# Performance work log

Hardware: AMD Instinct MI355X
Metric: run time of the kernel (lower is better)

Reference implementation:

```python
import jax, jax.numpy as jnp
import numpy as np
import math

B, N, DQK, DV, M = 8, 8192, 128, 128, 256


def _make_omega(m: int, d: int, seed: int = 0) -> jnp.ndarray:
    """Block-orthogonal random feature matrix, shape [d, m] (matches torch _omega)."""
    rng = np.random.default_rng(seed)
    blocks = []
    nblocks = m // d
    for _ in range(nblocks):
        q, _ = np.linalg.qr(rng.standard_normal((d, d)))
        blocks.append(q.T)
    missing = m - nblocks * d
    if missing > 0:
        q, _ = np.linalg.qr(rng.standard_normal((d, d)))
        blocks.append(q.T[:missing])
    norm = np.linalg.norm(rng.standard_normal((m, d)), axis=1, keepdims=True)
    omega = (norm * np.vstack(blocks)).T  # [d, m]
    return jnp.asarray(omega, dtype=jnp.float32)


def setup_inputs() -> dict:
    key = jax.random.key(0)
    kq, kk, kv = jax.random.split(key, 3)
    Q = jax.random.normal(kq, (B, N, DQK), jnp.float32)
    K = jax.random.normal(kk, (B, N, DQK), jnp.float32)
    V = jax.random.normal(kv, (B, N, DV), jnp.float32)
    atom_mask = jnp.ones((B, N), jnp.float32)
    omega = _make_omega(M, DQK)
    return {"Q": Q, "K": K, "V": V, "atom_mask": atom_mask, "omega": omega}


def _phi(X, mask, omega, is_query: bool, eps: float = 1e-4):
    """Project into random-feature space with Performer stabilization."""
    d = X.shape[-1]
    m = omega.shape[-1]
    U = (X / d ** 0.25) @ omega                       # [B, N, m]
    h = jnp.sum(X * X, axis=-1, keepdims=True) / (2.0 * d ** 0.5)
    if is_query:
        mx = jnp.max(U, axis=-1, keepdims=True)       # per-token max
    else:
        mx = jnp.max(U, axis=(-2, -1), keepdims=True)  # per-batch max
    return (jnp.exp(U - h - mx) + eps) / math.sqrt(m) * mask[..., None]


def reference(Q, K, V, atom_mask, omega):
    eps = 1e-8
    Qp = _phi(Q, atom_mask, omega, True)   # [B, N, M]
    Kp = _phi(K, atom_mask, omega, False)  # [B, N, M]
    # norm_n = Qp_n . sum_j Kp_j
    norm = jnp.einsum('bnm,bm->bn', Qp, jnp.sum(Kp, axis=1))[..., None] + eps
    KV = jnp.einsum('bnm,bnv->bmv', Kp, V)             # [B, M, DV]
    return jnp.einsum('bnm,bmv->bnv', Qp, KV) / norm   # [B, N, DV]
```

## Files before the change

kernel.cpp:

```cpp
#include <hip/hip_runtime.h>
#include <math.h>

#define BB 8
#define NN 8192
#define DD 128
#define MM 256
#define DVV 128
#define PP 32
#define CHUNK 32

#define XSCALE 0.29730177875068026f
#define INV_SQRT_M 0.0625f

typedef _Float16 f16x8 __attribute__((ext_vector_type(8)));
typedef float f32x16 __attribute__((ext_vector_type(16)));

#define FR(s, l) ((s) * 520 + (l) * 8)

__device__ __forceinline__ unsigned f2ord(float f) {
    unsigned u = __float_as_uint(f);
    return (u & 0x80000000u) ? ~u : (u | 0x80000000u);
}
__device__ __forceinline__ float ord2f(unsigned u) {
    return (u & 0x80000000u) ? __uint_as_float(u & 0x7fffffffu) : __uint_as_float(~u);
}
__device__ __forceinline__ f32x16 mfma16(f16x8 a, f16x8 b, f32x16 c) {
    return __builtin_amdgcn_mfma_f32_32x32x16_f16(a, b, c, 0, 0, 0);
}
__device__ __forceinline__ int rowf(int r, int q) { return (r & 3) + 8 * (r >> 2) + 4 * q; }

__device__ __forceinline__ void stage_A(const float* __restrict__ src,
                                        _Float16* R1, float* hs, float* msk,
                                        const float* __restrict__ mrow, bool do_h) {
    const int tid = threadIdx.x;
    const int t = tid >> 3, ks = tid & 7;
    const float4* s4 = (const float4*)(src + t * DD + ks * 16);
    float x[16];
    #pragma unroll
    for (int u = 0; u < 4; ++u) {
        float4 v = s4[u];
        x[u*4+0] = v.x * XSCALE; x[u*4+1] = v.y * XSCALE;
        x[u*4+2] = v.z * XSCALE; x[u*4+3] = v.w * XSCALE;
    }
    if (do_h) {
        float p = 0.f;
        #pragma unroll
        for (int u = 0; u < 16; ++u) p += x[u] * x[u];
        p += __shfl_xor(p, 1, 64); p += __shfl_xor(p, 2, 64); p += __shfl_xor(p, 4, 64);
        if (ks == 0) { hs[t] = 0.5f * p; msk[t] = mrow[t]; }
    }
    #pragma unroll
    for (int q = 0; q < 2; ++q) {
        f16x8 h8, l8;
        #pragma unroll
        for (int j = 0; j < 8; ++j) {
            float xv = x[q*8 + j];
            _Float16 h = (_Float16)xv;
            h8[j] = h; l8[j] = (_Float16)(xv - (float)h);
        }
        *(f16x8*)&R1[FR(0*8 + ks, q*32 + t)] = h8;
        *(f16x8*)&R1[FR(1*8 + ks, q*32 + t)] = l8;
    }
}

__device__ __forceinline__ void stage_BV(const float* __restrict__ src, _Float16* R1) {
    const int tid = threadIdx.x;
    const int t = tid >> 3, c0 = (tid & 7) * 16;
    const int ts = t >> 4, qq = (t >> 3) & 1, j = t & 7;
    const float4* s4 = (const float4*)(src + t * DVV + c0);
    #pragma unroll
    for (int u = 0; u < 4; ++u) {
        float4 v = s4[u];
        float vv[4] = {v.x, v.y, v.z, v.w};
        #pragma unroll
        for (int e = 0; e < 4; ++e) {
            int c = c0 + u*4 + e;
            int vt = c >> 5, iv = c & 31;
            _Float16 h = (_Float16)vv[e];
            R1[FR((0*4 + vt)*2 + ts, qq*32 + iv) + j] = h;
            R1[FR((1*4 + vt)*2 + ts, qq*32 + iv) + j] = (_Float16)(vv[e] - (float)h);
        }
    }
}

__global__ __launch_bounds__(256) void pack_kernel(const float* __restrict__ omega,
                                                   _Float16* __restrict__ omh,
                                                   _Float16* __restrict__ oml,
                                                   unsigned* __restrict__ kmaxord) {
    int g = blockIdx.x * 256 + threadIdx.x;
    if (g < BB) kmaxord[g] = f2ord(-INFINITY);
    int lane = g & 63, ks = (g >> 6) & 7, nt = g >> 9;
    int q = lane >> 5, i = lane & 31;
    f16x8 h8, l8;
    #pragma unroll
    for (int j = 0; j < 8; ++j) {
        float w = omega[(size_t)(ks*16 + q*8 + j) * MM + nt*32 + i];
        _Float16 h = (_Float16)w;
        h8[j] = h; l8[j] = (_Float16)(w - (float)h);
    }
    ((f16x8*)omh)[g] = h8;
    ((f16x8*)oml)[g] = l8;
}

__global__ __launch_bounds__(256) void kmax_kernel(const float* __restrict__ K,
                                                   const _Float16* __restrict__ omh,
                                                   unsigned* __restrict__ kmaxord) {
    __shared__ __align__(16) _Float16 R1[16 * 520];
    __shared__ float wred[4];
    const int b = blockIdx.y;
    const int tid = threadIdx.x, w = tid >> 6, lane = tid & 63;

    f16x8 om[2][8];
    #pragma unroll
    for (int n = 0; n < 2; ++n)
        #pragma unroll
        for (int k = 0; k < 8; ++k)
            om[n][k] = ((const f16x8*)omh)[((2*w + n)*8 + k)*64 + lane];

    float mx = -INFINITY;
    for (int c = 0; c < 4; ++c) {
        int t0 = (blockIdx.x * 4 + c) * CHUNK;
        __syncthreads();
        stage_A(K + ((size_t)b*NN + t0) * DD, R1, nullptr, nullptr, nullptr, false);
        __syncthreads();
        f32x16 a0, a1;
        #pragma unroll
        for (int r = 0; r < 16; ++r) { a0[r] = 0.f; a1[r] = 0.f; }
        #pragma unroll
        for (int ks = 0; ks < 8; ++ks) {
            f16x8 ah = *(const f16x8*)&R1[FR(ks, lane)];
            a0 = mfma16(ah, om[0][ks], a0);
            a1 = mfma16(ah, om[1][ks], a1);
        }
        #pragma unroll
        for (int r = 0; r < 16; ++r) mx = fmaxf(mx, fmaxf(a0[r], a1[r]));
    }
    #pragma unroll
    for (int off = 1; off < 64; off <<= 1) mx = fmaxf(mx, __shfl_xor(mx, off, 64));
    if (lane == 0) wred[w] = mx;
    __syncthreads();
    if (tid == 0)
        atomicMax(kmaxord + b,
                  f2ord(fmaxf(fmaxf(wred[0], wred[1]), fmaxf(wred[2], wred[3]))));
}

__global__ __launch_bounds__(256) void kv_kernel(const float* __restrict__ K,
                                                 const float* __restrict__ V,
                                                 const float* __restrict__ mask,
                                                 const _Float16* __restrict__ omh,
                                                 const _Float16* __restrict__ oml,
                                                 const unsigned* __restrict__ kmaxord,
                                                 float* __restrict__ pkv,
                                                 float* __restrict__ pks) {
    __shared__ __align__(16) _Float16 R1[16 * 520];
    __shared__ __align__(16) _Float16 R2[16 * 520];
    __shared__ float hs[32], msk[32];
    const int b = blockIdx.y, bx = blockIdx.x;
    const int rest = bx >> 3;
    const int h = rest & 1;
    const int p = (rest >> 1) * 8 + (bx & 7);
    const int tid = threadIdx.x, w = tid >> 6, lane = tid & 63;
    const int i = tid & 31, q = (tid >> 5) & 1;
    const int nt = h * 4 + w;
    const float kmaxv = ord2f(kmaxord[b]);

    f16x8 omf[2][8];
    #pragma unroll
    for (int k = 0; k < 8; ++k) {
        omf[0][k] = ((const f16x8*)omh)[(nt*8 + k)*64 + lane];
        omf[1][k] = ((const f16x8*)oml)[(nt*8 + k)*64 + lane];
    }

    f32x16 kvacc[4];
    #pragma unroll
    for (int vt = 0; vt < 4; ++vt)
        #pragma unroll
        for (int r = 0; r < 16; ++r) kvacc[vt][r] = 0.f;
    float ksa = 0.f;

    for (int c = 0; c < 8; ++c) {
        int t0 = (p * 8 + c) * CHUNK;
        __syncthreads();
        stage_A(K + ((size_t)b*NN + t0) * DD, R1, hs, msk,
                mask + (size_t)b*NN + t0, true);
        __syncthreads();

        f32x16 a0;
        #pragma unroll
        for (int r = 0; r < 16; ++r) a0[r] = 0.f;
        #pragma unroll
        for (int ks = 0; ks < 8; ++ks) {
            f16x8 ah = *(const f16x8*)&R1[FR(ks, lane)];
            f16x8 al = *(const f16x8*)&R1[FR(8 + ks, lane)];
            a0 = mfma16(ah, omf[0][ks], a0);
            a0 = mfma16(ah, omf[1][ks], a0);
            a0 = mfma16(al, omf[0][ks], a0);
        }
        __syncthreads();

        stage_BV(V + ((size_t)b*NN + t0) * DVV, R1);
        #pragma unroll
        for (int r = 0; r < 16; ++r) {
            int tok = rowf(r, q);
            float hh = hs[tok] + kmaxv;
            float mm = msk[tok] * INV_SQRT_M;
            float kp = (__expf(a0[r] - hh) + 1e-4f) * mm;
            ksa += kp;
            int ts = tok >> 4, qq = (tok >> 3) & 1, j = tok & 7;
            _Float16 hv = (_Float16)kp;
            R2[FR(w*2 + ts, qq*32 + i) + j] = hv;
            R2[FR(8 + w*2 + ts, qq*32 + i) + j] = (_Float16)(kp - (float)hv);
        }
        __syncthreads();

        f16x8 ah2[2], al2[2];
        #pragma unroll
        for (int ts = 0; ts < 2; ++ts) {
            ah2[ts] = *(const f16x8*)&R2[FR(w*2 + ts, lane)];
            al2[ts] = *(const f16x8*)&R2[FR(8 + w*2 + ts, lane)];
        }
        #pragma unroll
        for (int vt = 0; vt < 4; ++vt) {
            #pragma unroll
            for (int ts = 0; ts < 2; ++ts) {
                f16x8 bh = *(const f16x8*)&R1[FR(vt*2 + ts, lane)];
                f16x8 bl = *(const f16x8*)&R1[FR(8 + vt*2 + ts, lane)];
                kvacc[vt] = mfma16(ah2[ts], bh, kvacc[vt]);
                kvacc[vt] = mfma16(ah2[ts], bl, kvacc[vt]);
                kvacc[vt] = mfma16(al2[ts], bh, kvacc[vt]);
            }
        }
    }

    float* dst = pkv + ((size_t)(b * PP + p) << 15);
    #pragma unroll
    for (int vt = 0; vt < 4; ++vt)
        #pragma unroll
        for (int r = 0; r < 16; ++r) {
            int feat = nt*32 + rowf(r, q);
            dst[feat * DVV + vt*32 + i] = kvacc[vt][r];
        }
    {
        float s = ksa + __shfl_xor(ksa, 32, 64);
        if (q == 0) pks[(size_t)(b * PP + p) * MM + nt*32 + i] = s;
    }
}

__global__ __launch_bounds__(256) void reduce_kernel(const float* __restrict__ pkv,
                                                     const float* __restrict__ pks,
                                                     float* __restrict__ ksum,
                                                     _Float16* __restrict__ kvph,
                                                     _Float16* __restrict__ kvpl) {
    const int b = blockIdx.y;
    int g = blockIdx.x * 256 + threadIdx.x;
    float s = 0.f;
    for (int p = 0; p < PP; ++p) s += pkv[((size_t)(b * PP + p) << 15) + g];
    int f = g >> 7, v = g & 127;
    int vt = v >> 5, iv = v & 31, fs = f >> 4, qq = (f >> 3) & 1, j = f & 7;
    size_t idx = (size_t)b * 32768 + (size_t)((vt*16 + fs)*64 + qq*32 + iv)*8 + j;
    _Float16 h = (_Float16)s;
    kvph[idx] = h;
    kvpl[idx] = (_Float16)(s - (float)h);
    if (blockIdx.x == 0) {
        float ss = 0.f;
        for (int p = 0; p < PP; ++p) ss += pks[(size_t)(b * PP + p) * MM + g];
        ksum[b * MM + g] = ss;
    }
}

__global__ __launch_bounds__(256) void out_kernel(const float* __restrict__ Q,
                                                  const float* __restrict__ mask,
                                                  const _Float16* __restrict__ omh,
                                                  const _Float16* __restrict__ oml,
                                                  const float* __restrict__ ksum,
                                                  const _Float16* __restrict__ kvph,
                                                  const _Float16* __restrict__ kvpl,
                                                  float* __restrict__ out) {
    __shared__ __align__(16) _Float16 R1[16 * 520];
    __shared__ __align__(16) _Float16 R2[32 * 520];
    __shared__ float hs[32], msk[32], wmax[4][32], norms[32];
    const int b = blockIdx.y;
    const int tid = threadIdx.x, w = tid >> 6, lane = tid & 63;
    const int i = tid & 31, q = (tid >> 5) & 1;

    f16x8 omf[2][2][8];
    #pragma unroll
    for (int n = 0; n < 2; ++n)
        #pragma unroll
        for (int k = 0; k < 8; ++k) {
            omf[0][n][k] = ((const f16x8*)omh)[((2*w + n)*8 + k)*64 + lane];
            omf[1][n][k] = ((const f16x8*)oml)[((2*w + n)*8 + k)*64 + lane];
        }
    f16x8 bfh[16], bfl[16];
    #pragma unroll
    for (int fs = 0; fs < 16; ++fs) {
        bfh[fs] = ((const f16x8*)kvph)[(size_t)b * 4096 + (w*16 + fs)*64 + lane];
        bfl[fs] = ((const f16x8*)kvpl)[(size_t)b * 4096 + (w*16 + fs)*64 + lane];
    }
    f16x8 bnh[4], bnl[4];
    #pragma unroll
    for (int u = 0; u < 4; ++u) {
        f16x8 hh, ll;
        #pragma unroll
        for (int j = 0; j < 8; ++j) { hh[j] = (_Float16)0.f; ll[j] = (_Float16)0.f; }
        if (i == 0) {
            #pragma unroll
            for (int j = 0; j < 8; ++j) {
                float s = ksum[b * MM + (4*w + u)*16 + q*8 + j];
                _Float16 h = (_Float16)s;
                hh[j] = h; ll[j] = (_Float16)(s - (float)h);
            }
        }
        bnh[u] = hh; bnl[u] = ll;
    }

    for (int c = 0; c < 4; ++c) {
        int t0 = (blockIdx.x * 4 + c) * CHUNK;
        __syncthreads();
        stage_A(Q + ((size_t)b*NN + t0) * DD, R1, hs, msk,
                mask + (size_t)b*NN + t0, true);
        if (tid < 32) norms[tid] = 1e-8f;
        __syncthreads();

        f32x16 a0, a1;
        #pragma unroll
        for (int r = 0; r < 16; ++r) { a0[r] = 0.f; a1[r] = 0.f; }
        #pragma unroll
        for (int ks = 0; ks < 8; ++ks) {
            f16x8 ah = *(const f16x8*)&R1[FR(ks, lane)];
            f16x8 al = *(const f16x8*)&R1[FR(8 + ks, lane)];
            a0 = mfma16(ah, omf[0][0][ks], a0);
            a0 = mfma16(ah, omf[1][0][ks], a0);
            a0 = mfma16(al, omf[0][0][ks], a0);
            a1 = mfma16(ah, omf[0][1][ks], a1);
            a1 = mfma16(ah, omf[1][1][ks], a1);
            a1 = mfma16(al, omf[0][1][ks], a1);
        }
        float tm[16];
        #pragma unroll
        for (int r = 0; r < 16; ++r) tm[r] = fmaxf(a0[r], a1[r]);
        #pragma unroll
        for (int off = 1; off < 32; off <<= 1)
            #pragma unroll
            for (int r = 0; r < 16; ++r) tm[r] = fmaxf(tm[r], __shfl_xor(tm[r], off, 64));
        if (i == 0)
            #pragma unroll
            for (int r = 0; r < 16; ++r) wmax[w][rowf(r, q)] = tm[r];
        __syncthreads();

        #pragma unroll
        for (int r = 0; r < 16; ++r) {
            int tok = rowf(r, q);
            float tmax = fmaxf(fmaxf(wmax[0][tok], wmax[1][tok]),
                               fmaxf(wmax[2][tok], wmax[3][tok]));
            float hh = hs[tok] + tmax;
            float mm = msk[tok] * INV_SQRT_M;
            #pragma unroll
            for (int n = 0; n < 2; ++n) {
                float qp = (__expf((n ? a1[r] : a0[r]) - hh) + 1e-4f) * mm;
                int feat = (2*w + n)*32 + i;
                int fstep = feat >> 4, fq = (i >> 3) & 1, fj = i & 7;
                _Float16 h = (_Float16)qp;
                R2[FR(fstep, fq*32 + tok) + fj] = h;
                R2[FR(16 + fstep, fq*32 + tok) + fj] = (_Float16)(qp - (float)h);
            }
        }
        __syncthreads();

        f32x16 oa, na;
        #pragma unroll
        for (int r = 0; r < 16; ++r) { oa[r] = 0.f; na[r] = 0.f; }
        #pragma unroll
        for (int fs = 0; fs < 16; ++fs) {
            f16x8 ah = *(const f16x8*)&R2[FR(fs, lane)];
            f16x8 al = *(const f16x8*)&R2[FR(16 + fs, lane)];
            oa = mfma16(ah, bfh[fs], oa);
            oa = mfma16(ah, bfl[fs], oa);
            oa = mfma16(al, bfh[fs], oa);
        }
        #pragma unroll
        for (int u = 0; u < 4; ++u) {
            f16x8 ah = *(const f16x8*)&R2[FR(4*w + u, lane)];
            f16x8 al = *(const f16x8*)&R2[FR(16 + 4*w + u, lane)];
            na = mfma16(ah, bnh[u], na);
            na = mfma16(ah, bnl[u], na);
            na = mfma16(al, bnh[u], na);
        }
        if (i == 0)
            #pragma unroll
            for (int r = 0; r < 16; ++r) atomicAdd(&norms[rowf(r, q)], na[r]);
        __syncthreads();

        float* ob = out + ((size_t)b*NN + t0) * DVV + w*32 + i;
        #pragma unroll
        for (int r = 0; r < 16; ++r) {
            int tok = rowf(r, q);
            ob[(size_t)tok * DVV] = oa[r] * __builtin_amdgcn_rcpf(norms[tok]);
        }
    }
}

extern "C" void kernel_launch(void* const* d_in, const int* in_sizes, int n_in,
                              void* d_out, int out_size, void* d_ws, size_t ws_size,
                              hipStream_t stream) {
    const float* Q     = (const float*)d_in[0];
    const float* K     = (const float*)d_in[1];
    const float* V     = (const float*)d_in[2];
    const float* mask  = (const float*)d_in[3];
    const float* omega = (const float*)d_in[4];
    float* out = (float*)d_out;

    char* ws = (char*)d_ws;
    _Float16* omh    = (_Float16*)(ws);
    _Float16* oml    = (_Float16*)(ws + (64 << 10));
    unsigned* kmaxord = (unsigned*)(ws + (128 << 10));
    float*    ksum   = (float*)(ws + (132 << 10));
    float*    pks    = (float*)(ws + (140 << 10));
    _Float16* kvph   = (_Float16*)(ws + (400 << 10));
    _Float16* kvpl   = (_Float16*)(ws + (912 << 10));
    float*    pkv    = (float*)(ws + (2 << 20));

    pack_kernel<<<16, 256, 0, stream>>>(omega, omh, oml, kmaxord);
    kmax_kernel<<<dim3(64, BB), 256, 0, stream>>>(K, omh, kmaxord);
    kv_kernel<<<dim3(64, BB), 256, 0, stream>>>(K, V, mask, omh, oml, kmaxord, pkv, pks);
    reduce_kernel<<<dim3(128, BB), 256, 0, stream>>>(pkv, pks, ksum, kvph, kvpl);
    out_kernel<<<dim3(64, BB), 256, 0, stream>>>(Q, mask, omh, oml, ksum, kvph, kvpl, out);
}
```

Before: 247.1 us.

## Stream omega and KV fragments from global memory instead of holding them in registers

Drops the register-resident omega, KV and ksum fragment arrays in all three kernels. The B operands are now loaded from global/L2 memory inside non-unrolled, software-prefetched (double-buffered) MFMA loops, which should cut VGPR pressure and raise occupancy. In out_kernel the normalizer MFMA pass is replaced by a scalar dot product with ksum followed by a shuffle reduction, and one barrier is removed. The cost is repeated global loads on every chunk, plus less unrolling and less instruction-level parallelism.

```diff
diff --git a/kernel.cpp b/kernel.cpp
--- a/kernel.cpp
+++ b/kernel.cpp
@@ -109,15 +109,11 @@
     __shared__ float wred[4];
     const int b = blockIdx.y;
     const int tid = threadIdx.x, w = tid >> 6, lane = tid & 63;
-
-    f16x8 om[2][8];
-    #pragma unroll
-    for (int n = 0; n < 2; ++n)
-        #pragma unroll
-        for (int k = 0; k < 8; ++k)
-            om[n][k] = ((const f16x8*)omh)[((2*w + n)*8 + k)*64 + lane];
+    const int w2 = 2 * w;
+    const f16x8* OH = (const f16x8*)omh;
 
     float mx = -INFINITY;
+    #pragma unroll 1
     for (int c = 0; c < 4; ++c) {
         int t0 = (blockIdx.x * 4 + c) * CHUNK;
         __syncthreads();
@@ -126,11 +122,21 @@
         f32x16 a0, a1;
         #pragma unroll
         for (int r = 0; r < 16; ++r) { a0[r] = 0.f; a1[r] = 0.f; }
-        #pragma unroll
-        for (int ks = 0; ks < 8; ++ks) {
+        f16x8 X0 = OH[(w2*8 + 0)*64 + lane];
+        f16x8 X1 = OH[((w2+1)*8 + 0)*64 + lane];
+        #pragma unroll 1
+        for (int ks = 0; ks < 8; ks += 2) {
+            f16x8 Y0 = OH[(w2*8 + ks + 1)*64 + lane];
+            f16x8 Y1 = OH[((w2+1)*8 + ks + 1)*64 + lane];
             f16x8 ah = *(const f16x8*)&R1[FR(ks, lane)];
-            a0 = mfma16(ah, om[0][ks], a0);
-            a1 = mfma16(ah, om[1][ks], a1);
+            a0 = mfma16(ah, X0, a0);
+            a1 = mfma16(ah, X1, a1);
+            int k2 = (ks + 2) & 7;
+            X0 = OH[(w2*8 + k2)*64 + lane];
+            X1 = OH[((w2+1)*8 + k2)*64 + lane];
+            f16x8 ah2 = *(const f16x8*)&R1[FR(ks + 1, lane)];
+            a0 = mfma16(ah2, Y0, a0);
+            a1 = mfma16(ah2, Y1, a1);
         }
         #pragma unroll
         for (int r = 0; r < 16; ++r) mx = fmaxf(mx, fmaxf(a0[r], a1[r]));
@@ -163,13 +169,8 @@
     const int i = tid & 31, q = (tid >> 5) & 1;
     const int nt = h * 4 + w;
     const float kmaxv = ord2f(kmaxord[b]);
-
-    f16x8 omf[2][8];
-    #pragma unroll
-    for (int k = 0; k < 8; ++k) {
-        omf[0][k] = ((const f16x8*)omh)[(nt*8 + k)*64 + lane];
-        omf[1][k] = ((const f16x8*)oml)[(nt*8 + k)*64 + lane];
-    }
+    const f16x8* OH = (const f16x8*)omh;
+    const f16x8* OL = (const f16x8*)oml;
 
     f32x16 kvacc[4];
     #pragma unroll
@@ -178,6 +179,7 @@
         for (int r = 0; r < 16; ++r) kvacc[vt][r] = 0.f;
     float ksa = 0.f;
 
+    #pragma unroll 1
     for (int c = 0; c < 8; ++c) {
         int t0 = (p * 8 + c) * CHUNK;
         __syncthreads();
@@ -188,13 +190,25 @@
         f32x16 a0;
         #pragma unroll
         for (int r = 0; r < 16; ++r) a0[r] = 0.f;
-        #pragma unroll
-        for (int ks = 0; ks < 8; ++ks) {
+        f16x8 Xh = OH[(nt*8 + 0)*64 + lane];
+        f16x8 Xl = OL[(nt*8 + 0)*64 + lane];
+        #pragma unroll 1
+        for (int ks = 0; ks < 8; ks += 2) {
+            f16x8 Yh = OH[(nt*8 + ks + 1)*64 + lane];
+            f16x8 Yl = OL[(nt*8 + ks + 1)*64 + lane];
             f16x8 ah = *(const f16x8*)&R1[FR(ks, lane)];
             f16x8 al = *(const f16x8*)&R1[FR(8 + ks, lane)];
-            a0 = mfma16(ah, omf[0][ks], a0);
-            a0 = mfma16(ah, omf[1][ks], a0);
-            a0 = mfma16(al, omf[0][ks], a0);
+            a0 = mfma16(ah, Xh, a0);
+            a0 = mfma16(ah, Xl, a0);
+            a0 = mfma16(al, Xh, a0);
+            int k2 = (ks + 2) & 7;
+            Xh = OH[(nt*8 + k2)*64 + lane];
+            Xl = OL[(nt*8 + k2)*64 + lane];
+            f16x8 ah2 = *(const f16x8*)&R1[FR(ks + 1, lane)];
+            f16x8 al2 = *(const f16x8*)&R1[FR(8 + ks + 1, lane)];
+            a0 = mfma16(ah2, Yh, a0);
+            a0 = mfma16(ah2, Yl, a0);
+            a0 = mfma16(al2, Yh, a0);
         }
         __syncthreads();
 
@@ -282,38 +296,15 @@
     const int b = blockIdx.y;
     const int tid = threadIdx.x, w = tid >> 6, lane = tid & 63;
     const int i = tid & 31, q = (tid >> 5) & 1;
-
-    f16x8 omf[2][2][8];
-    #pragma unroll
-    for (int n = 0; n < 2; ++n)
-        #pragma unroll
-        for (int k = 0; k < 8; ++k) {
-            omf[0][n][k] = ((const f16x8*)omh)[((2*w + n)*8 + k)*64 + lane];
-            omf[1][n][k] = ((const f16x8*)oml)[((2*w + n)*8 + k)*64 + lane];
-        }
-    f16x8 bfh[16], bfl[16];
-    #pragma unroll
-    for (int fs = 0; fs < 16; ++fs) {
-        bfh[fs] = ((const f16x8*)kvph)[(size_t)b * 4096 + (w*16 + fs)*64 + lane];
-        bfl[fs] = ((const f16x8*)kvpl)[(size_t)b * 4096 + (w*16 + fs)*64 + lane];
-    }
-    f16x8 bnh[4], bnl[4];
-    #pragma unroll
-    for (int u = 0; u < 4; ++u) {
-        f16x8 hh, ll;
-        #pragma unroll
-        for (int j = 0; j < 8; ++j) { hh[j] = (_Float16)0.f; ll[j] = (_Float16)0.f; }
-        if (i == 0) {
-            #pragma unroll
-            for (int j = 0; j < 8; ++j) {
-                float s = ksum[b * MM + (4*w + u)*16 + q*8 + j];
-                _Float16 h = (_Float16)s;
-                hh[j] = h; ll[j] = (_Float16)(s - (float)h);
-            }
-        }
-        bnh[u] = hh; bnl[u] = ll;
-    }
-
+    const int w2 = 2 * w;
+    const f16x8* OH = (const f16x8*)omh;
+    const f16x8* OL = (const f16x8*)oml;
+    const f16x8* KH = (const f16x8*)kvph + (size_t)b * 4096 + (w*16)*64 + lane;
+    const f16x8* KL = (const f16x8*)kvpl + (size_t)b * 4096 + (w*16)*64 + lane;
+    const float nk0 = ksum[b * MM + w2*32 + i];
+    const float nk1 = ksum[b * MM + (w2+1)*32 + i];
+
+    #pragma unroll 1
     for (int c = 0; c < 4; ++c) {
         int t0 = (blockIdx.x * 4 + c) * CHUNK;
         __syncthreads();
@@ -325,17 +316,25 @@
         f32x16 a0, a1;
         #pragma unroll
         for (int r = 0; r < 16; ++r) { a0[r] = 0.f; a1[r] = 0.f; }
-        #pragma unroll
-        for (int ks = 0; ks < 8; ++ks) {
+        f16x8 X0h = OH[(w2*8 + 0)*64 + lane], X0l = OL[(w2*8 + 0)*64 + lane];
+        f16x8 X1h = OH[((w2+1)*8 + 0)*64 + lane], X1l = OL[((w2+1)*8 + 0)*64 + lane];
+        #pragma unroll 1
+        for (int ks = 0; ks < 8; ks += 2) {
+            f16x8 Y0h = OH[(w2*8 + ks + 1)*64 + lane], Y0l = OL[(w2*8 + ks + 1)*64 + lane];
+            f16x8 Y1h = OH[((w2+1)*8 + ks + 1)*64 + lane], Y1l = OL[((w2+1)*8 + ks + 1)*64 + lane];
             f16x8 ah = *(const f16x8*)&R1[FR(ks, lane)];
             f16x8 al = *(const f16x8*)&R1[FR(8 + ks, lane)];
-            a0 = mfma16(ah, omf[0][0][ks], a0);
-            a0 = mfma16(ah, omf[1][0][ks], a0);
-            a0 = mfma16(al, omf[0][0][ks], a0);
-            a1 = mfma16(ah, omf[0][1][ks], a1);
-            a1 = mfma16(ah, omf[1][1][ks], a1);
-            a1 = mfma16(al, omf[0][1][ks], a1);
-        }
+            a0 = mfma16(ah, X0h, a0); a0 = mfma16(ah, X0l, a0); a0 = mfma16(al, X0h, a0);
+            a1 = mfma16(ah, X1h, a1); a1 = mfma16(ah, X1l, a1); a1 = mfma16(al, X1h, a1);
+            int k2 = (ks + 2) & 7;
+            X0h = OH[(w2*8 + k2)*64 + lane]; X0l = OL[(w2*8 + k2)*64 + lane];
+            X1h = OH[((w2+1)*8 + k2)*64 + lane]; X1l = OL[((w2+1)*8 + k2)*64 + lane];
+            f16x8 ah2 = *(const f16x8*)&R1[FR(ks + 1, lane)];
+            f16x8 al2 = *(const f16x8*)&R1[FR(8 + ks + 1, lane)];
+            a0 = mfma16(ah2, Y0h, a0); a0 = mfma16(ah2, Y0l, a0); a0 = mfma16(al2, Y0h, a0);
+            a1 = mfma16(ah2, Y1h, a1); a1 = mfma16(ah2, Y1l, a1); a1 = mfma16(al2, Y1h, a1);
+        }
+
         float tm[16];
         #pragma unroll
         for (int r = 0; r < 16; ++r) tm[r] = fmaxf(a0[r], a1[r]);
@@ -348,6 +347,7 @@
             for (int r = 0; r < 16; ++r) wmax[w][rowf(r, q)] = tm[r];
         __syncthreads();
 
+        float nacc[16];
         #pragma unroll
         for (int r = 0; r < 16; ++r) {
             int tok = rowf(r, q);
@@ -355,41 +355,49 @@
                                fmaxf(wmax[2][tok], wmax[3][tok]));
             float hh = hs[tok] + tmax;
             float mm = msk[tok] * INV_SQRT_M;
+            float qp0 = (__expf(a0[r] - hh) + 1e-4f) * mm;
+            float qp1 = (__expf(a1[r] - hh) + 1e-4f) * mm;
+            nacc[r] = qp0 * nk0 + qp1 * nk1;
+            {
+                int feat = w2*32 + i;
+                int fstep = feat >> 4, fq = (i >> 3) & 1, fj = i & 7;
+                _Float16 hv = (_Float16)qp0;
+                R2[FR(fstep, fq*32 + tok) + fj] = hv;
+                R2[FR(16 + fstep, fq*32 + tok) + fj] = (_Float16)(qp0 - (float)hv);
+            }
+            {
+                int feat = (w2+1)*32 + i;
+                int fstep = feat >> 4, fq = (i >> 3) & 1, fj = i & 7;
+                _Float16 hv = (_Float16)qp1;
+                R2[FR(fstep, fq*32 + tok) + fj] = hv;
+                R2[FR(16 + fstep, fq*32 + tok) + fj] = (_Float16)(qp1 - (float)hv);
+            }
+        }
+        #pragma unroll
+        for (int off = 1; off < 32; off <<= 1)
             #pragma unroll
-            for (int n = 0; n < 2; ++n) {
-                float qp = (__expf((n ? a1[r] : a0[r]) - hh) + 1e-4f) * mm;
-                int feat = (2*w + n)*32 + i;
-                int fstep = feat >> 4, fq = (i >> 3) & 1, fj = i & 7;
-                _Float16 h = (_Float16)qp;
-                R2[FR(fstep, fq*32 + tok) + fj] = h;
-                R2[FR(16 + fstep, fq*32 + tok) + fj] = (_Float16)(qp - (float)h);
-            }
-        }
-        __syncthreads();
-
-        f32x16 oa, na;
-        #pragma unroll
-        for (int r = 0; r < 16; ++r) { oa[r] = 0.f; na[r] = 0.f; }
-        #pragma unroll
-        for (int fs = 0; fs < 16; ++fs) {
+            for (int r = 0; r < 16; ++r) nacc[r] += __shfl_xor(nacc[r], off, 64);
+        if (i == 0)
+            #pragma unroll
+            for (int r = 0; r < 16; ++r) atomicAdd(&norms[rowf(r, q)], nacc[r]);
+        __syncthreads();
+
+        f32x16 oa;
+        #pragma unroll
+        for (int r = 0; r < 16; ++r) oa[r] = 0.f;
+        f16x8 Fh = KH[0], Fl = KL[0];
+        #pragma unroll 1
+        for (int fs = 0; fs < 16; fs += 2) {
+            f16x8 Gh = KH[(fs + 1)*64], Gl = KL[(fs + 1)*64];
             f16x8 ah = *(const f16x8*)&R2[FR(fs, lane)];
             f16x8 al = *(const f16x8*)&R2[FR(16 + fs, lane)];
-            oa = mfma16(ah, bfh[fs], oa);
-            oa = mfma16(ah, bfl[fs], oa);
-            oa = mfma16(al, bfh[fs], oa);
-        }
-        #pragma unroll
-        for (int u = 0; u < 4; ++u) {
-            f16x8 ah = *(const f16x8*)&R2[FR(4*w + u, lane)];
-            f16x8 al = *(const f16x8*)&R2[FR(16 + 4*w + u, lane)];
-            na = mfma16(ah, bnh[u], na);
-            na = mfma16(ah, bnl[u], na);
-            na = mfma16(al, bnh[u], na);
-        }
-        if (i == 0)
-            #pragma unroll
-            for (int r = 0; r < 16; ++r) atomicAdd(&norms[rowf(r, q)], na[r]);
-        __syncthreads();
+            oa = mfma16(ah, Fh, oa); oa = mfma16(ah, Fl, oa); oa = mfma16(al, Fh, oa);
+            int f2 = (fs + 2) & 15;
+            Fh = KH[f2*64]; Fl = KL[f2*64];
+            f16x8 ah2 = *(const f16x8*)&R2[FR(fs + 1, lane)];
+            f16x8 al2 = *(const f16x8*)&R2[FR(16 + fs + 1, lane)];
+            oa = mfma16(ah2, Gh, oa); oa = mfma16(ah2, Gl, oa); oa = mfma16(al2, Gh, oa);
+        }
 
         float* ob = out + ((size_t)b*NN + t0) * DVV + w*32 + i;
         #pragma unroll
```

Measured after the change: 241.5 us (median of 2 runs). 2.3% less time.
